# Optimization experiments

Measured on AMD Instinct MI355X. Metric: run time of the kernel, lower is better.

The kernel has to match this reference:

```python
import jax, jax.numpy as jnp
import numpy as np

B, K, E, L, H, ENS = 32768, 5, 16, 128, 3, 3

def setup_inputs() -> dict:
    key = jax.random.key(0)
    ks = jax.random.split(key, 16)
    w = lambda i, shape: (jax.random.normal(ks[i], shape, jnp.float32) * 0.05)
    return {
        "z": jax.random.normal(ks[0], (B, L), jnp.float32),
        "anchors": jax.random.normal(ks[1], (B, K, 2), jnp.float32),
        # anchor_embed MLP: Linear(2,E) -> ReLU -> Linear(E,E)
        "W1": w(2, (E, 2)), "b1": w(3, (E,)),
        "W2": w(4, (E, E)), "b2": w(5, (E,)),
        # LSTMCell(E, L): gates order i,f,g,o
        "W_ih": w(6, (4 * L, E)), "W_hh": w(7, (4 * L, L)),
        "b_ih": w(8, (4 * L,)), "b_hh": w(9, (4 * L,)),
        # progress head Linear(L,1)
        "Wp": w(10, (1, L)), "bp": w(11, (1,)),
        # risk ensemble: ENS stacked Linear(L,1)
        "Wr": w(12, (ENS, L)), "br": w(13, (ENS,)),
    }

def reference(z, anchors, W1, b1, W2, b2, W_ih, W_hh, b_ih, b_hh, Wp, bp, Wr, br):
    Bc, Kc, _ = anchors.shape
    # anchor embedding MLP (B,K,2) -> (B,K,E)
    emb = jnp.maximum(anchors @ W1.T + b1, 0.0) @ W2.T + b2
    inp = emb.reshape(Bc * Kc, -1)                      # (B*K, E)
    h = jnp.broadcast_to(z[:, None, :], (Bc, Kc, z.shape[-1])).reshape(Bc * Kc, -1)
    c = jnp.zeros_like(h)
    x_proj = inp @ W_ih.T + b_ih                        # input projection constant over steps
    for _ in range(H):  # fixed small rollout horizon
        gates = x_proj + h @ W_hh.T + b_hh              # (B*K, 4L)
        i_g, f_g, g_g, o_g = jnp.split(gates, 4, axis=-1)
        i_g = jax.nn.sigmoid(i_g)
        f_g = jax.nn.sigmoid(f_g)
        g_g = jnp.tanh(g_g)
        o_g = jax.nn.sigmoid(o_g)
        c = f_g * c + i_g * g_g
        h = o_g * jnp.tanh(c)
    h = h.reshape(Bc, Kc, -1)                           # (B,K,L)
    progress = (h @ Wp.T + bp)[..., 0]                  # (B,K)
    risks = jnp.einsum('bkl,el->ebk', h, Wr) + br[:, None, None]  # (ENS,B,K)
    risk_mean = risks.mean(axis=0)
    unc = jnp.var(jax.nn.sigmoid(risks), axis=0, ddof=1)  # torch .var is unbiased
    return risk_mean, progress, unc, risks
```

## Files before the change

### kernel.cpp

```cpp
#include <hip/hip_runtime.h>

#define BN 32768
#define KN 5
#define LN 128
#define HN 3
#define ROWS (BN*KN)
#define BK ROWS
#define MT 64
#define TILES (ROWS/MT)
#define WGS 512
#define TPW (TILES/WGS)
#define THREADS 512
#define ASTR 168
#define LOG2E 1.44269504089f

using bf16x8 = __attribute__((ext_vector_type(8))) __bf16;
using bf16x2 = __attribute__((ext_vector_type(2))) __bf16;
using f32x4  = __attribute__((ext_vector_type(4))) float;
using u16x8  = __attribute__((ext_vector_type(8))) unsigned short;

__device__ inline unsigned short f2bf(float x) {
    union { float f; unsigned u; } v; v.f = x;
    unsigned r = v.u + 0x7FFFu + ((v.u >> 16) & 1u);
    return (unsigned short)(r >> 16);
}
#if __has_builtin(__builtin_amdgcn_cvt_pk_bf16_f32)
__device__ inline unsigned short f2bf_fast(float x) {
    union { bf16x2 v; unsigned short us[2]; } u;
    u.v = __builtin_amdgcn_cvt_pk_bf16_f32(x, x);
    return u.us[0];
}
#else
__device__ inline unsigned short f2bf_fast(float x) { return f2bf(x); }
#endif
__device__ inline float bf2f(unsigned short b) {
    union { unsigned u; float f; } v; v.u = ((unsigned)b) << 16; return v.f;
}
__device__ inline float sigm(float x) {
    return __builtin_amdgcn_rcpf(1.0f + __builtin_amdgcn_exp2f(-LOG2E * x));
}
__device__ inline f32x4 splat4(float x) { f32x4 r; r[0]=x; r[1]=x; r[2]=x; r[3]=x; return r; }

#define POINTWISE(MTI) do {                                                        \
    _Pragma("unroll")                                                              \
    for (int r_ = 0; r_ < 4; ++r_) {                                               \
        const float Ei = __builtin_amdgcn_exp2f(acc[MTI][0][r_]);       \
        const float Ef = __builtin_amdgcn_exp2f(acc[MTI][1][r_]);       \
        const float Eg = __builtin_amdgcn_exp2f(acc[MTI][2][r_]);       \
        const float Eo = __builtin_amdgcn_exp2f(acc[MTI][3][r_]);       \
        const float t1  = (1.0f + Ei) * (1.0f + Eg);                               \
        const float ef1 = 1.0f + Ef;                                               \
        const float t3  = (Eg - 1.0f) * ef1;                                       \
        const float num = fmaf(cst[(MTI)*4 + r_], t1, t3);                         \
        const float cn  = num * __builtin_amdgcn_rcpf(t1 * ef1);                   \
        cst[(MTI)*4 + r_] = cn;                                                    \
        const float Ec = __builtin_amdgcn_exp2f(2.0f * LOG2E * cn);                \
        const float hn = (Ec - 1.0f) *                                             \
            __builtin_amdgcn_rcpf((1.0f + Eo) * (1.0f + Ec));                      \
        sA[nxt * MT * ASTR + ((MTI)*16 + quad*4 + r_) * ASTR + 16 + lcol] =        \
            f2bf_fast(hn);                                                         \
    }                                                                              \
} while (0)

__global__ __launch_bounds__(THREADS, 2)
void wahead_kernel(const float* __restrict__ z,   const float* __restrict__ anchors,
                   const float* __restrict__ W1,  const float* __restrict__ b1,
                   const float* __restrict__ W2,  const float* __restrict__ b2,
                   const float* __restrict__ Wih, const float* __restrict__ Whh,
                   const float* __restrict__ bih, const float* __restrict__ bhh,
                   const float* __restrict__ Wp,  const float* __restrict__ bp,
                   const float* __restrict__ Wr,  const float* __restrict__ br,
                   float* __restrict__ out)
{
    __shared__ unsigned short sA[2 * MT * ASTR];
    __shared__ float sW1[32], sb1[16], sW2[16 * 17], sb2[16], sWp[128], sWr[384];

    const int tid  = threadIdx.x;
    const int wv   = tid >> 6;
    const int lane = tid & 63;
    const int quad = lane >> 4;
    const int cc   = lane & 15;
    const int lcol = wv * 16 + cc;

    if (tid < 32)  sW1[tid] = W1[tid];
    if (tid < 16)  { sb1[tid] = b1[tid]; sb2[tid] = b2[tid]; }
    if (tid < 256) sW2[(tid >> 4) * 17 + (tid & 15)] = W2[tid];
    if (tid < 128) sWp[tid] = Wp[tid];
    if (tid < 384) sWr[tid] = Wr[tid];

    bf16x8 Bf[4][5];
    float  biasv[4];
    #pragma unroll
    for (int t = 0; t < 4; ++t) {
        const float sc = (t == 2) ? (2.0f * LOG2E) : (-LOG2E);
        const int n = t * 128 + wv * 16 + cc;
        biasv[t] = sc * (bih[n] + bhh[n]);
        #pragma unroll
        for (int kt = 0; kt < 5; ++kt) {
            const int k0 = kt * 32 + quad * 8;
            float v[8];
            if (k0 < 16) {
                const float4 p0 = *reinterpret_cast<const float4*>(Wih + n * 16 + k0);
                const float4 p1 = *reinterpret_cast<const float4*>(Wih + n * 16 + k0 + 4);
                v[0]=p0.x; v[1]=p0.y; v[2]=p0.z; v[3]=p0.w;
                v[4]=p1.x; v[5]=p1.y; v[6]=p1.z; v[7]=p1.w;
            } else if (k0 < 144) {
                const float4 p0 = *reinterpret_cast<const float4*>(Whh + n * 128 + (k0 - 16));
                const float4 p1 = *reinterpret_cast<const float4*>(Whh + n * 128 + (k0 - 16) + 4);
                v[0]=p0.x; v[1]=p0.y; v[2]=p0.z; v[3]=p0.w;
                v[4]=p1.x; v[5]=p1.y; v[6]=p1.z; v[7]=p1.w;
            } else {
                #pragma unroll
                for (int j = 0; j < 8; ++j) v[j] = 0.0f;
            }
            union { bf16x8 bv; unsigned short us[8]; } pk;
            #pragma unroll
            for (int j = 0; j < 8; ++j) pk.us[j] = f2bf(sc * v[j]);
            Bf[t][kt] = pk.bv;
        }
    }

    const float bpv = bp[0];
    const float br0 = br[0], br1 = br[1], br2 = br[2];

    __syncthreads();

    const int erow = tid >> 3;
    const int esub = tid & 7;

    float  pax, pay;
    float4 pz0, pz1, pz2, pz3;
    {
        const int gr = blockIdx.x * TPW * MT + erow;
        const float2 an = *reinterpret_cast<const float2*>(anchors + gr * 2);
        pax = an.x; pay = an.y;
        const unsigned b_idx = (unsigned)gr / 5u;
        const float4* zp = reinterpret_cast<const float4*>(z + (size_t)b_idx * 128 + esub * 16);
        pz0 = zp[0]; pz1 = zp[1]; pz2 = zp[2]; pz3 = zp[3];
    }

    #pragma unroll 1
    for (int ti = 0; ti < TPW; ++ti) {
        const int tile = blockIdx.x * TPW + ti;
        const int r0g  = tile * MT;

        {
            const float ax = pax, ay = pay;
            const int e0 = esub * 2;
            float a0 = sb2[e0], a1 = sb2[e0 + 1];
            #pragma unroll
            for (int hh = 0; hh < 16; ++hh) {
                float pre = fmaf(sW1[hh * 2], ax, fmaf(sW1[hh * 2 + 1], ay, sb1[hh]));
                pre = fmaxf(pre, 0.0f);
                a0 = fmaf(pre, sW2[e0 * 17 + hh], a0);
                a1 = fmaf(pre, sW2[(e0 + 1) * 17 + hh], a1);
            }
            const unsigned short b0 = f2bf(a0), b1v = f2bf(a1);
            #pragma unroll
            for (int bufi = 0; bufi < 2; ++bufi) {
                unsigned short* row = &sA[bufi * MT * ASTR + erow * ASTR];
                row[e0]       = b0;  row[e0 + 1]       = b1v;
                row[144 + e0] = 0;   row[144 + e0 + 1] = 0;
            }
            union { u16x8 v; unsigned short us[8]; } w0, w1;
            w0.us[0]=f2bf(pz0.x); w0.us[1]=f2bf(pz0.y); w0.us[2]=f2bf(pz0.z); w0.us[3]=f2bf(pz0.w);
            w0.us[4]=f2bf(pz1.x); w0.us[5]=f2bf(pz1.y); w0.us[6]=f2bf(pz1.z); w0.us[7]=f2bf(pz1.w);
            w1.us[0]=f2bf(pz2.x); w1.us[1]=f2bf(pz2.y); w1.us[2]=f2bf(pz2.z); w1.us[3]=f2bf(pz2.w);
            w1.us[4]=f2bf(pz3.x); w1.us[5]=f2bf(pz3.y); w1.us[6]=f2bf(pz3.z); w1.us[7]=f2bf(pz3.w);
            unsigned short* hrow = &sA[erow * ASTR + 16 + esub * 16];
            *reinterpret_cast<u16x8*>(hrow)     = w0.v;
            *reinterpret_cast<u16x8*>(hrow + 8) = w1.v;
        }

        float cst[16];
        #pragma unroll
        for (int e = 0; e < 16; ++e) cst[e] = 0.0f;

        #pragma unroll
        for (int s = 0; s < HN; ++s) {
            const int cur = s & 1;
            const int nxt = cur ^ 1;
            __syncthreads();

            if (s == HN - 1 && ti + 1 < TPW) {
                const int gr = (r0g + MT) + erow;
                const float2 an = *reinterpret_cast<const float2*>(anchors + gr * 2);
                pax = an.x; pay = an.y;
                const unsigned b_idx = (unsigned)gr / 5u;
                const float4* zp = reinterpret_cast<const float4*>(z + (size_t)b_idx * 128 + esub * 16);
                pz0 = zp[0]; pz1 = zp[1]; pz2 = zp[2]; pz3 = zp[3];
            }

            f32x4 acc[4][4];
            #pragma unroll
            for (int mt = 0; mt < 4; ++mt)
                #pragma unroll
                for (int t = 0; t < 4; ++t)
                    acc[mt][t] = splat4(biasv[t]);

            bf16x8 af[2][5];
            #pragma unroll
            for (int kt = 0; kt < 5; ++kt)
                af[0][kt] = *reinterpret_cast<const bf16x8*>(
                    &sA[cur * MT * ASTR + cc * ASTR + kt * 32 + quad * 8]);
            #pragma unroll
            for (int mt = 0; mt < 4; ++mt) {
                const int pb = mt & 1;
                if (mt < 3) {
                    #pragma unroll
                    for (int kt = 0; kt < 5; ++kt)
                        af[pb ^ 1][kt] = *reinterpret_cast<const bf16x8*>(
                            &sA[cur * MT * ASTR + ((mt + 1) * 16 + cc) * ASTR + kt * 32 + quad * 8]);
                }
                #pragma unroll
                for (int kt = 0; kt < 5; ++kt)
                    #pragma unroll
                    for (int t = 0; t < 4; ++t)
                        acc[mt][t] = __builtin_amdgcn_mfma_f32_16x16x32_bf16(
                            af[pb][kt], Bf[t][kt], acc[mt][t], 0, 0, 0);
                if (mt == 1) POINTWISE(0);
                else if (mt == 2) POINTWISE(1);
                else if (mt == 3) POINTWISE(2);
            }
            POINTWISE(3);
        }

        __syncthreads();

        {
            const int row = tid >> 3;
            const int j   = tid & 7;
            const unsigned short* hrow = &sA[1 * MT * ASTR + row * ASTR + 16 + j * 16];
            const u16x8 h0 = *reinterpret_cast<const u16x8*>(hrow);
            const u16x8 h1 = *reinterpret_cast<const u16x8*>(hrow + 8);
            float p = 0.f, q0 = 0.f, q1 = 0.f, q2 = 0.f;
            #pragma unroll
            for (int u = 0; u < 16; ++u) {
                const int l = j * 16 + u;
                const float hv = bf2f(u < 8 ? h0[u] : h1[u - 8]);
                p  = fmaf(hv, sWp[l], p);
                q0 = fmaf(hv, sWr[l], q0);
                q1 = fmaf(hv, sWr[128 + l], q1);
                q2 = fmaf(hv, sWr[256 + l], q2);
            }
            #pragma unroll
            for (int m = 1; m < 8; m <<= 1) {
                p  += __shfl_xor(p,  m, 64);
                q0 += __shfl_xor(q0, m, 64);
                q1 += __shfl_xor(q1, m, 64);
                q2 += __shfl_xor(q2, m, 64);
            }
            if (j == 0) {
                const int gr = r0g + row;
                const float prog  = p + bpv;
                const float rr0 = q0 + br0, rr1 = q1 + br1, rr2 = q2 + br2;
                const float rmean = (rr0 + rr1 + rr2) * (1.0f / 3.0f);
                const float s0 = sigm(rr0), s1 = sigm(rr1), s2 = sigm(rr2);
                const float sm = (s0 + s1 + s2) * (1.0f / 3.0f);
                const float d0 = s0 - sm, d1 = s1 - sm, d2 = s2 - sm;
                const float unc = (d0 * d0 + d1 * d1 + d2 * d2) * 0.5f;
                out[gr]          = rmean;
                out[BK + gr]     = prog;
                out[2 * BK + gr] = unc;
                out[3 * BK + gr] = rr0;
                out[4 * BK + gr] = rr1;
                out[5 * BK + gr] = rr2;
            }
        }
    }
}

extern "C" void kernel_launch(void* const* d_in, const int* in_sizes, int n_in,
                              void* d_out, int out_size, void* d_ws, size_t ws_size,
                              hipStream_t stream) {
    const float* z       = (const float*)d_in[0];
    const float* anchors = (const float*)d_in[1];
    const float* W1      = (const float*)d_in[2];
    const float* b1      = (const float*)d_in[3];
    const float* W2      = (const float*)d_in[4];
    const float* b2      = (const float*)d_in[5];
    const float* Wih     = (const float*)d_in[6];
    const float* Whh     = (const float*)d_in[7];
    const float* bih     = (const float*)d_in[8];
    const float* bhh     = (const float*)d_in[9];
    const float* Wp      = (const float*)d_in[10];
    const float* bp      = (const float*)d_in[11];
    const float* Wr      = (const float*)d_in[12];
    const float* br      = (const float*)d_in[13];

    hipLaunchKernelGGL(wahead_kernel, dim3(WGS), dim3(THREADS), 0, stream,
                       z, anchors, W1, b1, W2, b2, Wih, Whh, bih, bhh,
                       Wp, bp, Wr, br, (float*)d_out);
}
```

Before: 213.7 us.

## Batch LSTM pointwise gate math after all MFMAs instead of interleaving

Moves the LSTM cell pointwise update out of the MFMA loop. Previously each 16-row tile's gates were processed while the next tile's MFMAs ran. Now all four tiles' MFMAs are issued first, and the pointwise work follows in two batches of eight elements, grouped by stage (exp, cell update, tanh, store). This gives more independent transcendental work per stage to hide latency. In exchange it gives up the overlap between matrix-core and vector work, and holding more temporaries in flight raises register pressure.

Measured after the change: 215.7 us. About the same (+0.9%).

```diff
diff --git a/kernel.cpp b/kernel.cpp
--- a/kernel.cpp
+++ b/kernel.cpp
@@ -41,23 +41,37 @@
 }
 __device__ inline f32x4 splat4(float x) { f32x4 r; r[0]=x; r[1]=x; r[2]=x; r[3]=x; return r; }
 
-#define POINTWISE(MTI) do {                                                        \
+#define PW_BATCH(B_) do {                                                          \
+    float Ei_[8], Ef_[8], Eg_[8], Eo_[8];                                          \
     _Pragma("unroll")                                                              \
-    for (int r_ = 0; r_ < 4; ++r_) {                                               \
-        const float Ei = __builtin_amdgcn_exp2f(acc[MTI][0][r_]);       \
-        const float Ef = __builtin_amdgcn_exp2f(acc[MTI][1][r_]);       \
-        const float Eg = __builtin_amdgcn_exp2f(acc[MTI][2][r_]);       \
-        const float Eo = __builtin_amdgcn_exp2f(acc[MTI][3][r_]);       \
-        const float t1  = (1.0f + Ei) * (1.0f + Eg);                               \
-        const float ef1 = 1.0f + Ef;                                               \
-        const float t3  = (Eg - 1.0f) * ef1;                                       \
-        const float num = fmaf(cst[(MTI)*4 + r_], t1, t3);                         \
-        const float cn  = num * __builtin_amdgcn_rcpf(t1 * ef1);                   \
-        cst[(MTI)*4 + r_] = cn;                                                    \
-        const float Ec = __builtin_amdgcn_exp2f(2.0f * LOG2E * cn);                \
-        const float hn = (Ec - 1.0f) *                                             \
-            __builtin_amdgcn_rcpf((1.0f + Eo) * (1.0f + Ec));                      \
-        sA[nxt * MT * ASTR + ((MTI)*16 + quad*4 + r_) * ASTR + 16 + lcol] =        \
+    for (int j_ = 0; j_ < 8; ++j_) {                                               \
+        const int mt_ = 2*(B_) + (j_ >> 2), r_ = j_ & 3;                           \
+        Ei_[j_] = __builtin_amdgcn_exp2f(acc[mt_][0][r_]);             \
+        Ef_[j_] = __builtin_amdgcn_exp2f(acc[mt_][1][r_]);             \
+        Eg_[j_] = __builtin_amdgcn_exp2f(acc[mt_][2][r_]);             \
+        Eo_[j_] = __builtin_amdgcn_exp2f(acc[mt_][3][r_]);             \
+    }                                                                              \
+    float cn_[8];                                                                  \
+    _Pragma("unroll")                                                              \
+    for (int j_ = 0; j_ < 8; ++j_) {                                               \
+        const int e_ = (B_)*8 + j_;                                                \
+        const float t1  = (1.0f + Ei_[j_]) * (1.0f + Eg_[j_]);                     \
+        const float ef1 = 1.0f + Ef_[j_];                                          \
+        const float t3  = (Eg_[j_] - 1.0f) * ef1;                                  \
+        const float num = fmaf(cst[e_], t1, t3);                                   \
+        cn_[j_] = num * __builtin_amdgcn_rcpf(t1 * ef1);                           \
+        cst[e_] = cn_[j_];                                                         \
+    }                                                                              \
+    float Ec_[8];                                                                  \
+    _Pragma("unroll")                                                              \
+    for (int j_ = 0; j_ < 8; ++j_)                                                 \
+        Ec_[j_] = __builtin_amdgcn_exp2f(2.0f * LOG2E * cn_[j_]);                  \
+    _Pragma("unroll")                                                              \
+    for (int j_ = 0; j_ < 8; ++j_) {                                               \
+        const int mt_ = 2*(B_) + (j_ >> 2), r_ = j_ & 3;                           \
+        const float hn = (Ec_[j_] - 1.0f) *                                        \
+            __builtin_amdgcn_rcpf((1.0f + Eo_[j_]) * (1.0f + Ec_[j_]));            \
+        sA[nxt * MT * ASTR + (mt_*16 + quad*4 + r_) * ASTR + 16 + lcol] =          \
             f2bf_fast(hn);                                                         \
     }                                                                              \
 } while (0)
@@ -218,11 +232,10 @@
                     for (int t = 0; t < 4; ++t)
                         acc[mt][t] = __builtin_amdgcn_mfma_f32_16x16x32_bf16(
                             af[pb][kt], Bf[t][kt], acc[mt][t], 0, 0, 0);
-                if (mt == 1) POINTWISE(0);
-                else if (mt == 2) POINTWISE(1);
-                else if (mt == 3) POINTWISE(2);
-            }
-            POINTWISE(3);
+            }
+
+            PW_BATCH(0);
+            PW_BATCH(1);
         }
 
         __syncthreads();
```

## Double tile rows per block and restructure MFMA loop with two rotating accumulators

Applied to the files above, without the earlier changes.

Doubles the tile height from 64 to 128 rows and halves the grid to 256 blocks, so each block processes larger tiles with fewer barriers per row. The MFMA loop now walks 8 row sub-tiles using only two ping-pong accumulator sets, with each sub-tile's LSTM pointwise work interleaved after the next sub-tile's MFMAs. Precomputed LDS read/write base pointers replace the per-access index math, and bf16 packing now converts two values per call. In exchange, the prefetch of the next tile's anchors and z is dropped, so those loads are exposed, and the larger LDS footprint and per-thread cell state may hurt occupancy.

New measurement: 196.0 us, median of 2. 1.09x faster.

```diff
diff --git a/kernel.cpp b/kernel.cpp
--- a/kernel.cpp
+++ b/kernel.cpp
@@ -6,9 +6,9 @@
 #define HN 3
 #define ROWS (BN*KN)
 #define BK ROWS
-#define MT 64
+#define MT 128
 #define TILES (ROWS/MT)
-#define WGS 512
+#define WGS 256
 #define TPW (TILES/WGS)
 #define THREADS 512
 #define ASTR 168
@@ -30,8 +30,16 @@
     u.v = __builtin_amdgcn_cvt_pk_bf16_f32(x, x);
     return u.us[0];
 }
+__device__ inline unsigned pk2bf(float lo, float hi) {
+    union { bf16x2 v; unsigned u; } q;
+    q.v = __builtin_amdgcn_cvt_pk_bf16_f32(lo, hi);
+    return q.u;
+}
 #else
 __device__ inline unsigned short f2bf_fast(float x) { return f2bf(x); }
+__device__ inline unsigned pk2bf(float lo, float hi) {
+    return (unsigned)f2bf(lo) | ((unsigned)f2bf(hi) << 16);
+}
 #endif
 __device__ inline float bf2f(unsigned short b) {
     union { unsigned u; float f; } v; v.u = ((unsigned)b) << 16; return v.f;
@@ -41,13 +49,13 @@
 }
 __device__ inline f32x4 splat4(float x) { f32x4 r; r[0]=x; r[1]=x; r[2]=x; r[3]=x; return r; }
 
-#define POINTWISE(MTI) do {                                                        \
+#define PW_MT(ACCI, MTI, WB_) do {                                                 \
     _Pragma("unroll")                                                              \
     for (int r_ = 0; r_ < 4; ++r_) {                                               \
-        const float Ei = __builtin_amdgcn_exp2f(acc[MTI][0][r_]);       \
-        const float Ef = __builtin_amdgcn_exp2f(acc[MTI][1][r_]);       \
-        const float Eg = __builtin_amdgcn_exp2f(acc[MTI][2][r_]);       \
-        const float Eo = __builtin_amdgcn_exp2f(acc[MTI][3][r_]);       \
+        const float Ei = __builtin_amdgcn_exp2f(acc[ACCI][0][r_]);      \
+        const float Ef = __builtin_amdgcn_exp2f(acc[ACCI][1][r_]);      \
+        const float Eg = __builtin_amdgcn_exp2f(acc[ACCI][2][r_]);      \
+        const float Eo = __builtin_amdgcn_exp2f(acc[ACCI][3][r_]);      \
         const float t1  = (1.0f + Ei) * (1.0f + Eg);                               \
         const float ef1 = 1.0f + Ef;                                               \
         const float t3  = (Eg - 1.0f) * ef1;                                       \
@@ -57,8 +65,7 @@
         const float Ec = __builtin_amdgcn_exp2f(2.0f * LOG2E * cn);                \
         const float hn = (Ec - 1.0f) *                                             \
             __builtin_amdgcn_rcpf((1.0f + Eo) * (1.0f + Ec));                      \
-        sA[nxt * MT * ASTR + ((MTI)*16 + quad*4 + r_) * ASTR + 16 + lcol] =        \
-            f2bf_fast(hn);                                                         \
+        (WB_)[(MTI)*16*ASTR + r_*ASTR] = f2bf_fast(hn);                            \
     }                                                                              \
 } while (0)
 
@@ -125,19 +132,15 @@
 
     __syncthreads();
 
-    const int erow = tid >> 3;
-    const int esub = tid & 7;
-
-    float  pax, pay;
-    float4 pz0, pz1, pz2, pz3;
-    {
-        const int gr = blockIdx.x * TPW * MT + erow;
-        const float2 an = *reinterpret_cast<const float2*>(anchors + gr * 2);
-        pax = an.x; pay = an.y;
-        const unsigned b_idx = (unsigned)gr / 5u;
-        const float4* zp = reinterpret_cast<const float4*>(z + (size_t)b_idx * 128 + esub * 16);
-        pz0 = zp[0]; pz1 = zp[1]; pz2 = zp[2]; pz3 = zp[3];
-    }
+    const int erow = tid >> 2;
+    const int esub = tid & 3;
+
+    const unsigned short* rbB[2];
+    unsigned short*       wbB[2];
+    rbB[0] = &sA[0 * MT * ASTR + cc * ASTR + quad * 8];
+    rbB[1] = &sA[1 * MT * ASTR + cc * ASTR + quad * 8];
+    wbB[0] = &sA[0 * MT * ASTR + (quad * 4) * ASTR + 16 + lcol];
+    wbB[1] = &sA[1 * MT * ASTR + (quad * 4) * ASTR + 16 + lcol];
 
     #pragma unroll 1
     for (int ti = 0; ti < TPW; ++ti) {
@@ -145,36 +148,50 @@
         const int r0g  = tile * MT;
 
         {
-            const float ax = pax, ay = pay;
-            const int e0 = esub * 2;
-            float a0 = sb2[e0], a1 = sb2[e0 + 1];
+            const int gr = r0g + erow;
+            const float2 an = *reinterpret_cast<const float2*>(anchors + gr * 2);
+            const int e0 = esub * 4;
+            float a0 = sb2[e0], a1 = sb2[e0 + 1], a2 = sb2[e0 + 2], a3 = sb2[e0 + 3];
             #pragma unroll
             for (int hh = 0; hh < 16; ++hh) {
-                float pre = fmaf(sW1[hh * 2], ax, fmaf(sW1[hh * 2 + 1], ay, sb1[hh]));
+                float pre = fmaf(sW1[hh * 2], an.x, fmaf(sW1[hh * 2 + 1], an.y, sb1[hh]));
                 pre = fmaxf(pre, 0.0f);
                 a0 = fmaf(pre, sW2[e0 * 17 + hh], a0);
                 a1 = fmaf(pre, sW2[(e0 + 1) * 17 + hh], a1);
-            }
-            const unsigned short b0 = f2bf(a0), b1v = f2bf(a1);
+                a2 = fmaf(pre, sW2[(e0 + 2) * 17 + hh], a2);
+                a3 = fmaf(pre, sW2[(e0 + 3) * 17 + hh], a3);
+            }
+            const unsigned ep0 = pk2bf(a0, a1), ep1 = pk2bf(a2, a3);
             #pragma unroll
             for (int bufi = 0; bufi < 2; ++bufi) {
                 unsigned short* row = &sA[bufi * MT * ASTR + erow * ASTR];
-                row[e0]       = b0;  row[e0 + 1]       = b1v;
-                row[144 + e0] = 0;   row[144 + e0 + 1] = 0;
-            }
-            union { u16x8 v; unsigned short us[8]; } w0, w1;
-            w0.us[0]=f2bf(pz0.x); w0.us[1]=f2bf(pz0.y); w0.us[2]=f2bf(pz0.z); w0.us[3]=f2bf(pz0.w);
-            w0.us[4]=f2bf(pz1.x); w0.us[5]=f2bf(pz1.y); w0.us[6]=f2bf(pz1.z); w0.us[7]=f2bf(pz1.w);
-            w1.us[0]=f2bf(pz2.x); w1.us[1]=f2bf(pz2.y); w1.us[2]=f2bf(pz2.z); w1.us[3]=f2bf(pz2.w);
-            w1.us[4]=f2bf(pz3.x); w1.us[5]=f2bf(pz3.y); w1.us[6]=f2bf(pz3.z); w1.us[7]=f2bf(pz3.w);
-            unsigned short* hrow = &sA[erow * ASTR + 16 + esub * 16];
-            *reinterpret_cast<u16x8*>(hrow)     = w0.v;
-            *reinterpret_cast<u16x8*>(hrow + 8) = w1.v;
+                *reinterpret_cast<unsigned*>(&row[e0])       = ep0;
+                *reinterpret_cast<unsigned*>(&row[e0 + 2])   = ep1;
+                *reinterpret_cast<unsigned*>(&row[144 + e0]) = 0u;
+                *reinterpret_cast<unsigned*>(&row[144 + e0 + 2]) = 0u;
+            }
+            const unsigned b_idx = (unsigned)gr / 5u;
+            const float* zb = z + (size_t)b_idx * 128 + esub * 32;
+            unsigned short* hrow = &sA[erow * ASTR + 16 + esub * 32];
+            #pragma unroll
+            for (int c = 0; c < 2; ++c) {
+                const float4 q0 = *reinterpret_cast<const float4*>(zb + c * 16);
+                const float4 q1 = *reinterpret_cast<const float4*>(zb + c * 16 + 4);
+                const float4 q2 = *reinterpret_cast<const float4*>(zb + c * 16 + 8);
+                const float4 q3 = *reinterpret_cast<const float4*>(zb + c * 16 + 12);
+                union { u16x8 v; unsigned u32[4]; } w0, w1;
+                w0.u32[0] = pk2bf(q0.x, q0.y); w0.u32[1] = pk2bf(q0.z, q0.w);
+                w0.u32[2] = pk2bf(q1.x, q1.y); w0.u32[3] = pk2bf(q1.z, q1.w);
+                w1.u32[0] = pk2bf(q2.x, q2.y); w1.u32[1] = pk2bf(q2.z, q2.w);
+                w1.u32[2] = pk2bf(q3.x, q3.y); w1.u32[3] = pk2bf(q3.z, q3.w);
+                *reinterpret_cast<u16x8*>(hrow + c * 16)     = w0.v;
+                *reinterpret_cast<u16x8*>(hrow + c * 16 + 8) = w1.v;
+            }
         }
 
-        float cst[16];
+        float cst[32];
         #pragma unroll
-        for (int e = 0; e < 16; ++e) cst[e] = 0.0f;
+        for (int e = 0; e < 32; ++e) cst[e] = 0.0f;
 
         #pragma unroll
         for (int s = 0; s < HN; ++s) {
@@ -182,69 +199,66 @@
             const int nxt = cur ^ 1;
             __syncthreads();
 
-            if (s == HN - 1 && ti + 1 < TPW) {
-                const int gr = (r0g + MT) + erow;
-                const float2 an = *reinterpret_cast<const float2*>(anchors + gr * 2);
-                pax = an.x; pay = an.y;
-                const unsigned b_idx = (unsigned)gr / 5u;
-                const float4* zp = reinterpret_cast<const float4*>(z + (size_t)b_idx * 128 + esub * 16);
-                pz0 = zp[0]; pz1 = zp[1]; pz2 = zp[2]; pz3 = zp[3];
-            }
-
-            f32x4 acc[4][4];
-            #pragma unroll
-            for (int mt = 0; mt < 4; ++mt)
+            const unsigned short* rb = rbB[cur];
+            unsigned short*       wb = wbB[nxt];
+
+            f32x4 acc[2][4];
+            bf16x8 af[2][5];
+            #pragma unroll
+            for (int kt = 0; kt < 5; ++kt)
+                af[0][kt] = *reinterpret_cast<const bf16x8*>(rb + kt * 32);
+
+            #pragma unroll
+            for (int mt = 0; mt < 8; ++mt) {
+                const int pb = mt & 1;
                 #pragma unroll
                 for (int t = 0; t < 4; ++t)
-                    acc[mt][t] = splat4(biasv[t]);
-
-            bf16x8 af[2][5];
-            #pragma unroll
-            for (int kt = 0; kt < 5; ++kt)
-                af[0][kt] = *reinterpret_cast<const bf16x8*>(
-                    &sA[cur * MT * ASTR + cc * ASTR + kt * 32 + quad * 8]);
-            #pragma unroll
-            for (int mt = 0; mt < 4; ++mt) {
-                const int pb = mt & 1;
-                if (mt < 3) {
+                    acc[pb][t] = splat4(biasv[t]);
+                if (mt < 7) {
                     #pragma unroll
                     for (int kt = 0; kt < 5; ++kt)
                         af[pb ^ 1][kt] = *reinterpret_cast<const bf16x8*>(
-                            &sA[cur * MT * ASTR + ((mt + 1) * 16 + cc) * ASTR + kt * 32 + quad * 8]);
+                            rb + (mt + 1) * 16 * ASTR + kt * 32);
                 }
                 #pragma unroll
                 for (int kt = 0; kt < 5; ++kt)
                     #pragma unroll
                     for (int t = 0; t < 4; ++t)
-                        acc[mt][t] = __builtin_amdgcn_mfma_f32_16x16x32_bf16(
-                            af[pb][kt], Bf[t][kt], acc[mt][t], 0, 0, 0);
-                if (mt == 1) POINTWISE(0);
-                else if (mt == 2) POINTWISE(1);
-                else if (mt == 3) POINTWISE(2);
-            }
-            POINTWISE(3);
+                        acc[pb][t] = __builtin_amdgcn_mfma_f32_16x16x32_bf16(
+                            af[pb][kt], Bf[t][kt], acc[pb][t], 0, 0, 0);
+                if (mt == 1) PW_MT(0, 0, wb);
+                else if (mt == 2) PW_MT(1, 1, wb);
+                else if (mt == 3) PW_MT(0, 2, wb);
+                else if (mt == 4) PW_MT(1, 3, wb);
+                else if (mt == 5) PW_MT(0, 4, wb);
+                else if (mt == 6) PW_MT(1, 5, wb);
+                else if (mt == 7) PW_MT(0, 6, wb);
+            }
+            PW_MT(1, 7, wb);
         }
 
         __syncthreads();
 
         {
-            const int row = tid >> 3;
-            const int j   = tid & 7;
-            const unsigned short* hrow = &sA[1 * MT * ASTR + row * ASTR + 16 + j * 16];
-            const u16x8 h0 = *reinterpret_cast<const u16x8*>(hrow);
-            const u16x8 h1 = *reinterpret_cast<const u16x8*>(hrow + 8);
+            const int row = tid >> 2;
+            const int j   = tid & 3;
+            const unsigned short* hrow = &sA[1 * MT * ASTR + row * ASTR + 16 + j * 32];
             float p = 0.f, q0 = 0.f, q1 = 0.f, q2 = 0.f;
             #pragma unroll
-            for (int u = 0; u < 16; ++u) {
-                const int l = j * 16 + u;
-                const float hv = bf2f(u < 8 ? h0[u] : h1[u - 8]);
-                p  = fmaf(hv, sWp[l], p);
-                q0 = fmaf(hv, sWr[l], q0);
-                q1 = fmaf(hv, sWr[128 + l], q1);
-                q2 = fmaf(hv, sWr[256 + l], q2);
-            }
-            #pragma unroll
-            for (int m = 1; m < 8; m <<= 1) {
+            for (int c = 0; c < 4; ++c) {
+                const u16x8 hv8 = *reinterpret_cast<const u16x8*>(hrow + c * 8);
+                #pragma unroll
+                for (int u = 0; u < 8; ++u) {
+                    const int l = j * 32 + c * 8 + u;
+                    const float hv = bf2f(hv8[u]);
+                    p  = fmaf(hv, sWp[l], p);
+                    q0 = fmaf(hv, sWr[l], q0);
+                    q1 = fmaf(hv, sWr[128 + l], q1);
+                    q2 = fmaf(hv, sWr[256 + l], q2);
+                }
+            }
+            #pragma unroll
+            for (int m = 1; m < 4; m <<= 1) {
                 p  += __shfl_xor(p,  m, 64);
                 q0 += __shfl_xor(q0, m, 64);
                 q1 += __shfl_xor(q1, m, 64);
```
